# Kernel optimization log

Hardware: AMD Instinct MI355X
Metric: run time of the kernel (lower is better)

Reference implementation:

```python
import jax, jax.numpy as jnp
import numpy as np

N_NODES = 50000
N_EDGES = 800000
N_GRAPHS = 64
FEAT = 128
HID = 256
ACT = 32


def setup_inputs() -> dict:
    key = jax.random.key(0)
    ks = jax.random.split(key, 16)
    x = jax.random.normal(ks[0], (N_NODES, FEAT), dtype=jnp.float32)
    edge_index = jax.random.randint(ks[1], (2, N_EDGES), 0, N_NODES, dtype=jnp.int32)
    # sorted graph assignment covering all graphs (avoids empty segments in mean pool)
    batch = (jnp.arange(N_NODES, dtype=jnp.int32) * N_GRAPHS) // N_NODES
    action = jax.random.normal(ks[2], (N_GRAPHS, ACT), dtype=jnp.float32)

    def lin(k, fan_in, fan_out):
        s = 1.0 / np.sqrt(fan_in)
        kw, kb = jax.random.split(k)
        W = jax.random.uniform(kw, (fan_in, fan_out), jnp.float32, -s, s)
        b = jax.random.uniform(kb, (fan_out,), jnp.float32, -s, s)
        return W, b

    q1_W1, q1_b1 = lin(ks[3], FEAT, HID)
    q1_W2, q1_b2 = lin(ks[4], HID, HID)
    q1_fcW, q1_fcb = lin(ks[5], HID + ACT, 1)
    q2_W1, q2_b1 = lin(ks[6], FEAT, HID)
    q2_W2, q2_b2 = lin(ks[7], HID, HID)
    q2_fcW, q2_fcb = lin(ks[8], HID + ACT, 1)
    return dict(x=x, edge_index=edge_index, batch=batch, action=action,
                q1_W1=q1_W1, q1_b1=q1_b1, q1_W2=q1_W2, q1_b2=q1_b2,
                q1_fcW=q1_fcW, q1_fcb=q1_fcb,
                q2_W1=q2_W1, q2_b1=q2_b1, q2_W2=q2_W2, q2_b2=q2_b2,
                q2_fcW=q2_fcW, q2_fcb=q2_fcb)


def _gcn_conv(x, W, b, src, dst, norm, n_nodes):
    # GCNConv: h = D^-1/2 (A+I) D^-1/2 (x W) + b
    h = x @ W                                    # [N, out]
    msg = h[src] * norm[:, None]                 # [E+N, out] gather
    out = jax.ops.segment_sum(msg, dst, num_segments=n_nodes)  # scatter-add
    return out + b


def _critic_head(x, src, dst, norm, batch, action, W1, b1, W2, b2, fcW, fcb, counts):
    n = x.shape[0]
    h = jax.nn.relu(_gcn_conv(x, W1, b1, src, dst, norm, n))
    h = jax.nn.relu(_gcn_conv(h, W2, b2, src, dst, norm, n))
    pooled = jax.ops.segment_sum(h, batch, num_segments=N_GRAPHS) / counts[:, None]
    q_in = jnp.concatenate([pooled, action], axis=-1)
    return q_in @ fcW + fcb


def reference(x, edge_index, batch, action,
              q1_W1, q1_b1, q1_W2, q1_b2, q1_fcW, q1_fcb,
              q2_W1, q2_b1, q2_W2, q2_b2, q2_fcW, q2_fcb):
    n = x.shape[0]
    # add self-loops (PyG GCNConv default)
    loops = jnp.arange(n, dtype=edge_index.dtype)
    src = jnp.concatenate([edge_index[0], loops])
    dst = jnp.concatenate([edge_index[1], loops])
    deg = jax.ops.segment_sum(jnp.ones_like(dst, x.dtype), dst, num_segments=n)
    dis = jnp.where(deg > 0, jax.lax.rsqrt(deg), 0.0)
    norm = dis[src] * dis[dst]                   # symmetric normalization per edge
    counts = jax.ops.segment_sum(jnp.ones_like(batch, x.dtype), batch,
                                 num_segments=N_GRAPHS)
    q1 = _critic_head(x, src, dst, norm, batch, action,
                      q1_W1, q1_b1, q1_W2, q1_b2, q1_fcW, q1_fcb, counts)
    q2 = _critic_head(x, src, dst, norm, batch, action,
                      q2_W1, q2_b1, q2_W2, q2_b2, q2_fcW, q2_fcb, counts)
    return (q1, q2)
```

## Files before the change

### kernel.cpp

```cpp
#include <hip/hip_runtime.h>
#include <hip/hip_bf16.h>

#define FEAT 128
#define HID  256
#define ACTD 32

typedef __attribute__((ext_vector_type(8))) short bf16x8;
typedef __attribute__((ext_vector_type(4))) float f32x4;
typedef __attribute__((ext_vector_type(2))) float f32x2;

__device__ __forceinline__ ushort f2b(float f) {
    __hip_bfloat16 h = __float2bfloat16(f);
    return *(ushort*)&h;
}
__device__ __forceinline__ uint pack2(float lo, float hi) {
    return (uint)f2b(lo) | ((uint)f2b(hi) << 16);
}
__device__ __forceinline__ f32x2 upk_lo(uint u) { return __builtin_amdgcn_cvt_pk_f32_fp8(u, false); }
__device__ __forceinline__ f32x2 upk_hi(uint u) { return __builtin_amdgcn_cvt_pk_f32_fp8(u, true); }

__device__ __forceinline__ void add8(float* acc, uint2 g) {
    f32x2 l0 = upk_lo(g.x), h0 = upk_hi(g.x);
    f32x2 l1 = upk_lo(g.y), h1 = upk_hi(g.y);
    acc[0] += l0[0]; acc[1] += l0[1]; acc[2] += h0[0]; acc[3] += h0[1];
    acc[4] += l1[0]; acc[5] += l1[1]; acc[6] += h1[0]; acc[7] += h1[1];
}


__global__ void hist_bounds(const int* __restrict__ dst, int* __restrict__ cnt, int E,
                            const int* __restrict__ batch, int* __restrict__ sg,
                            int* __restrict__ eg, int n) {
    int i = blockIdx.x * blockDim.x + threadIdx.x;
    if (i < E) atomicAdd(&cnt[dst[i]], 1);
    if (i < n) {
        int b = batch[i];
        if (i == 0 || batch[i - 1] != b) sg[b] = i;
        if (i == n - 1 || batch[i + 1] != b) eg[b] = i + 1;
    }
}

__global__ __launch_bounds__(256) void scan_one(const int* __restrict__ cnt,
        int* __restrict__ row_ptr, int* __restrict__ row_end,
        int* __restrict__ fill_pos, float* __restrict__ dis,
        int* __restrict__ ticket, int n) {
    __shared__ int s[256];
    __shared__ int base_sh;
    int t = threadIdx.x;
    int i = blockIdx.x * 256 + t;
    int c = (i < n) ? cnt[i] : 0;
    s[t] = c;
    __syncthreads();
    for (int off = 1; off < 256; off <<= 1) {
        int u = (t >= off) ? s[t - off] : 0;
        __syncthreads();
        s[t] += u;
        __syncthreads();
    }
    if (t == 255) base_sh = atomicAdd(ticket, s[255]);
    __syncthreads();
    if (i < n) {
        int ex = base_sh + s[t] - c;
        row_ptr[i] = ex;
        row_end[i] = ex + c;
        fill_pos[i] = ex;
        dis[i] = rsqrtf((float)c + 1.0f);
    }
}

__global__ void fill_prep(const int* __restrict__ src, const int* __restrict__ dst,
                          int* __restrict__ fill_pos, int* __restrict__ col_idx, int E,
                          const float* __restrict__ x, const float* __restrict__ dis,
                          uchar* __restrict__ xs,
                          const float* __restrict__ W1a, const float* __restrict__ W1b,
                          const float* __restrict__ W2a, const float* __restrict__ W2b,
                          ushort* __restrict__ WT1, uchar* __restrict__ WT2f, int n) {
    int i = blockIdx.x * blockDim.x + threadIdx.x;
    if (i < E) {
        int d = dst[i];
        int pos = atomicAdd(&fill_pos[d], 1);
        col_idx[pos] = src[i];
        return;
    }
    i -= E;
    const int nscale = n * (FEAT / 4);
    if (i < nscale) {
        int v = i >> 5;
        float dv = dis[v] * 8.f;
        float4 f = ((const float4*)x)[i];
        uint p = __builtin_amdgcn_cvt_pk_fp8_f32(f.x * dv, f.y * dv, 0, false);
        p = __builtin_amdgcn_cvt_pk_fp8_f32(f.z * dv, f.w * dv, p, true);
        ((uint*)xs)[i] = p;
        return;
    }
    i -= nscale;
    if (i < 2 * FEAT * HID) {
        int head = i >> 15;
        int rem = i & 32767;
        int k = rem >> 8, nn = rem & 255;
        const float* W = head ? W1b : W1a;
        WT1[(size_t)(head * 256 + nn) * FEAT + k] = f2b(W[rem]);
    } else {
        int j = i - 2 * FEAT * HID;
        if (j >= 2 * HID * HID) return;
        int head = j >> 16;
        int rem = j & 65535;
        int k = rem >> 8, nn = rem & 255;
        const float* W = head ? W2b : W2a;
        float v = W[rem] * 8.f;
        uint q = __builtin_amdgcn_cvt_pk_fp8_f32(v, v, 0, false);
        WT2f[(size_t)head * 65536 + nn * 256 + k] = (uchar)(q & 0xff);
    }
}


__global__ __launch_bounds__(256) void agg128(
        const uchar* __restrict__ xs, const float* __restrict__ dis,
        const int* __restrict__ row_ptr, const int* __restrict__ row_end,
        const int* __restrict__ col_idx,
        ushort* __restrict__ z, int n) {
    const int wave = threadIdx.x >> 6, lane = threadIdx.x & 63;
    const int v = blockIdx.x * 4 + wave;
    if (v >= n) return;
    const ushort* X = (const ushort*)xs;
    f32x2 p = upk_lo((uint)X[(size_t)v * 64 + lane]);
    float a0 = p[0], a1 = p[1];
    const int e0 = row_ptr[v], e1 = row_end[v];
    int e = e0;
    for (; e + 8 <= e1; e += 8) {
        uint m[8];
#pragma unroll
        for (int j = 0; j < 8; ++j) m[j] = X[(size_t)col_idx[e + j] * 64 + lane];
#pragma unroll
        for (int j = 0; j < 8; ++j) {
            f32x2 q = upk_lo(m[j]);
            a0 += q[0]; a1 += q[1];
        }
    }
    for (; e < e1; ++e) {
        f32x2 m = upk_lo((uint)X[(size_t)col_idx[e] * 64 + lane]);
        a0 += m[0]; a1 += m[1];
    }
    float sc = dis[v] * 0.125f;
    ((uint*)z)[(size_t)v * 64 + lane] = pack2(a0 * sc, a1 * sc);
}


__global__ __launch_bounds__(256) void agg512(
        const uchar* __restrict__ h1, const float* __restrict__ dis,
        const int* __restrict__ row_ptr, const int* __restrict__ row_end,
        const int* __restrict__ col_idx,
        uchar* __restrict__ z2f, int n) {
    const int wave = threadIdx.x >> 6, lane = threadIdx.x & 63;
    const int v = blockIdx.x * 4 + wave;
    if (v >= n) return;
    const uint2* H = (const uint2*)h1;
    float acc[8];
    {
        uint2 g = H[(size_t)v * 64 + lane];
        f32x2 l0 = upk_lo(g.x), h0 = upk_hi(g.x);
        f32x2 l1 = upk_lo(g.y), h1v = upk_hi(g.y);
        acc[0] = l0[0]; acc[1] = l0[1]; acc[2] = h0[0]; acc[3] = h0[1];
        acc[4] = l1[0]; acc[5] = l1[1]; acc[6] = h1v[0]; acc[7] = h1v[1];
    }
    const int e0 = row_ptr[v], e1 = row_end[v];
    int e = e0;
    for (; e + 8 <= e1; e += 8) {
        uint2 m[8];
#pragma unroll
        for (int j = 0; j < 8; ++j) m[j] = H[(size_t)col_idx[e + j] * 64 + lane];
#pragma unroll
        for (int j = 0; j < 8; ++j) add8(acc, m[j]);
    }
    for (; e < e1; ++e) add8(acc, H[(size_t)col_idx[e] * 64 + lane]);
    float sc = dis[v] * 0.25f;
    uint lo = __builtin_amdgcn_cvt_pk_fp8_f32(acc[0] * sc, acc[1] * sc, 0, false);
    lo = __builtin_amdgcn_cvt_pk_fp8_f32(acc[2] * sc, acc[3] * sc, lo, true);
    uint hi = __builtin_amdgcn_cvt_pk_fp8_f32(acc[4] * sc, acc[5] * sc, 0, false);
    hi = __builtin_amdgcn_cvt_pk_fp8_f32(acc[6] * sc, acc[7] * sc, hi, true);
    uint2 o = {lo, hi};
    ((uint2*)z2f)[(size_t)v * 64 + lane] = o;
}


__global__ __launch_bounds__(512) void gemm1_mfma(
        const ushort* __restrict__ z,
        const ushort* __restrict__ WT1,
        const float* __restrict__ b1a, const float* __restrict__ b1b,
        const float* __restrict__ dis,
        uchar* __restrict__ out, int M) {
    constexpr int K = FEAT;
    __shared__ char Bs[256 * 256];
    const int tid = threadIdx.x;
    const int bm = blockIdx.x * 128;
    const int head = blockIdx.y;
    const ushort* WT = WT1 + (size_t)head * 256 * K;
    const float* bias = head ? b1b : b1a;

    for (int idx = tid; idx < 256 * 16; idx += 512) {
        int nr = idx >> 4, seg = idx & 15;
        int4 val = *(const int4*)(WT + (size_t)nr * K + seg * 8);
        int byte = (nr * 256 + seg * 16) ^ ((nr & 7) << 4);
        *(int4*)(Bs + byte) = val;
    }
    __syncthreads();

    const int warp = tid >> 6, lane = tid & 63;
    const int wr = warp >> 1, wc = warp & 1;
    const int kgrp = lane >> 4;
    const int r0 = wr * 32 + (lane & 15);
    const int c0 = wc * 128 + (lane & 15);

    f32x4 acc[2][8] = {};
    const bf16x8 zv = {};
    for (int ks = 0; ks < 4; ++ks) {
        bf16x8 a[2], b[8];
#pragma unroll
        for (int m = 0; m < 2; ++m) {
            int grow = bm + r0 + m * 16;
            a[m] = (grow < M)
                 ? *(const bf16x8*)(z + (size_t)grow * K + ks * 32 + kgrp * 8)
                 : zv;
        }
#pragma unroll
        for (int nf = 0; nf < 8; ++nf) {
            int nr = c0 + nf * 16;
            int byte = (nr * 256 + ks * 64 + kgrp * 16) ^ ((nr & 7) << 4);
            b[nf] = *(const bf16x8*)(Bs + byte);
        }
#pragma unroll
        for (int nf = 0; nf < 8; ++nf)
#pragma unroll
            for (int m = 0; m < 2; ++m)
                acc[m][nf] = __builtin_amdgcn_mfma_f32_16x16x32_bf16(b[nf], a[m], acc[m][nf], 0, 0, 0);
    }

    const int ml = lane & 15;
    const int ngrp = (lane >> 4) * 4;
#pragma unroll
    for (int m = 0; m < 2; ++m) {
        int grow = bm + wr * 32 + m * 16 + ml;
        if (grow >= M) continue;
        float d = dis[grow] * 16.f;
#pragma unroll
        for (int nf = 0; nf < 8; ++nf) {
            int n0 = wc * 128 + nf * 16 + ngrp;
            float4 bv = *(const float4*)(bias + n0);
            f32x4 ac = acc[m][nf];
            float v0 = fmaxf(ac[0] + bv.x, 0.f) * d;
            float v1 = fmaxf(ac[1] + bv.y, 0.f) * d;
            float v2 = fmaxf(ac[2] + bv.z, 0.f) * d;
            float v3 = fmaxf(ac[3] + bv.w, 0.f) * d;
            uint q = __builtin_amdgcn_cvt_pk_fp8_f32(v0, v1, 0, false);
            q = __builtin_amdgcn_cvt_pk_fp8_f32(v2, v3, q, true);
            *(uint*)(out + (size_t)grow * 512 + head * 256 + n0) = q;
        }
    }
}


__global__ __launch_bounds__(512) void gemm2_pool(
        const uchar* __restrict__ z2f,
        const uchar* __restrict__ WT2f,
        const float* __restrict__ b2a, const float* __restrict__ b2b,
        const int* __restrict__ batch,
        float* __restrict__ pooled, int M) {
    constexpr int K = HID;
    __shared__ char Bs[256 * 256];
    __shared__ int rows_g[128];
    const int tid = threadIdx.x;
    const int bm = blockIdx.x * 128;
    const int head = blockIdx.y;
    const uchar* WT = WT2f + (size_t)head * 65536;
    const float* bias = head ? b2b : b2a;

    for (int idx = tid; idx < 256 * 32; idx += 512) {
        int nr = idx >> 5, seg = idx & 31;
        uint2 val = *(const uint2*)(WT + (size_t)nr * 256 + seg * 8);
        int byte = (nr * 256 + seg * 8) ^ ((nr & 7) << 3);
        *(uint2*)(Bs + byte) = val;
    }
    if (tid < 128) rows_g[tid] = batch[min(bm + tid, M - 1)];
    __syncthreads();

    const int warp = tid >> 6, lane = tid & 63;
    const int wr = warp >> 1, wc = warp & 1;
    const int kgrp = lane >> 4;
    const int r0 = wr * 32 + (lane & 15);
    const int c0 = wc * 128 + (lane & 15);
    const uchar* Abase = z2f + (size_t)head * 256;

    f32x4 acc[2][8] = {};
    for (int ks = 0; ks < 8; ++ks) {
        long a[2], b[8];
#pragma unroll
        for (int m = 0; m < 2; ++m) {
            int grow = bm + r0 + m * 16;
            a[m] = (grow < M)
                 ? *(const long*)(Abase + (size_t)grow * 512 + ks * 32 + kgrp * 8)
                 : 0L;
        }
#pragma unroll
        for (int nf = 0; nf < 8; ++nf) {
            int nr = c0 + nf * 16;
            int byte = (nr * 256 + ks * 32 + kgrp * 8) ^ ((nr & 7) << 3);
            b[nf] = *(const long*)(Bs + byte);
        }
#pragma unroll
        for (int nf = 0; nf < 8; ++nf)
#pragma unroll
            for (int m = 0; m < 2; ++m)
                acc[m][nf] = __builtin_amdgcn_mfma_f32_16x16x32_fp8_fp8(a[m], b[nf], acc[m][nf], 0, 0, 0);
    }

    const int rbw = wr * 32;
    const int g0 = rows_g[rbw];
    const int glast = rows_g[min(127, rbw + 31)];
    float s0[8] = {}, s1[8] = {};
#pragma unroll
    for (int m = 0; m < 2; ++m) {
#pragma unroll
        for (int r = 0; r < 4; ++r) {
            int lrow = rbw + m * 16 + (lane >> 4) * 4 + r;
            int grow = bm + lrow;
            if (grow < M) {
                bool in0 = (rows_g[lrow] == g0);
#pragma unroll
                for (int nf = 0; nf < 8; ++nf) {
                    float val = fmaxf(acc[m][nf][r] * 0.03125f + bias[c0 + nf * 16], 0.f);
                    if (in0) s0[nf] += val; else s1[nf] += val;
                }
            }
        }
    }
#pragma unroll
    for (int nf = 0; nf < 8; ++nf) {
        s0[nf] += __shfl_xor(s0[nf], 16, 64);
        s0[nf] += __shfl_xor(s0[nf], 32, 64);
        s1[nf] += __shfl_xor(s1[nf], 16, 64);
        s1[nf] += __shfl_xor(s1[nf], 32, 64);
    }
    if (kgrp == 0) {
#pragma unroll
        for (int nf = 0; nf < 8; ++nf) {
            int n = head * 256 + c0 + nf * 16;
            atomicAdd(&pooled[(size_t)g0 * 512 + n], s0[nf]);
            if (glast != g0) atomicAdd(&pooled[(size_t)glast * 512 + n], s1[nf]);
        }
    }
}

__global__ __launch_bounds__(512) void final_dot(
        const float* __restrict__ pooled, const int* __restrict__ sg,
        const int* __restrict__ eg, const float* __restrict__ action,
        const float* __restrict__ fcW1, const float* __restrict__ fcb1,
        const float* __restrict__ fcW2, const float* __restrict__ fcb2,
        float* __restrict__ out, int G) {
    int g = blockIdx.x, t = threadIdx.x;
    int head = t >> 8, f = t & 255;
    const float* fcW = head ? fcW2 : fcW1;
    float inv = 1.f / (float)(eg[g] - sg[g]);
    float p = pooled[g * 512 + t] * inv * fcW[f];
    if (f < ACTD) p += action[g * ACTD + f] * fcW[HID + f];
    for (int off = 32; off; off >>= 1) p += __shfl_down(p, off, 64);
    __shared__ float red[8];
    if ((t & 63) == 0) red[t >> 6] = p;
    __syncthreads();
    if (t == 0)   out[g]     = red[0] + red[1] + red[2] + red[3] + fcb1[0];
    if (t == 256) out[G + g] = red[4] + red[5] + red[6] + red[7] + fcb2[0];
}


extern "C" void kernel_launch(void* const* d_in, const int* in_sizes, int n_in,
                              void* d_out, int out_size, void* d_ws, size_t ws_size,
                              hipStream_t stream) {
    const float* x      = (const float*)d_in[0];
    const int*   ei     = (const int*)d_in[1];
    const int*   batch  = (const int*)d_in[2];
    const float* action = (const float*)d_in[3];
    const float* q1_W1  = (const float*)d_in[4];
    const float* q1_b1  = (const float*)d_in[5];
    const float* q1_W2  = (const float*)d_in[6];
    const float* q1_b2  = (const float*)d_in[7];
    const float* q1_fcW = (const float*)d_in[8];
    const float* q1_fcb = (const float*)d_in[9];
    const float* q2_W1  = (const float*)d_in[10];
    const float* q2_b1  = (const float*)d_in[11];
    const float* q2_W2  = (const float*)d_in[12];
    const float* q2_b2  = (const float*)d_in[13];
    const float* q2_fcW = (const float*)d_in[14];
    const float* q2_fcb = (const float*)d_in[15];

    const int N = in_sizes[2];
    const int E = in_sizes[1] / 2;
    const int G = in_sizes[3] / ACTD;
    const int* src = ei;
    const int* dst = ei + E;

    char* w = (char*)d_ws;
    size_t off = 0;
    auto take = [&](size_t bytes) -> void* {
        void* p = w + off;
        off = (off + bytes + 255) & ~(size_t)255;
        return p;
    };
    int*    cnt      = (int*)take((size_t)(N + 1) * 4);
    int*    row_ptr  = (int*)take((size_t)N * 4);
    int*    row_end  = (int*)take((size_t)N * 4);
    int*    fill_pos = (int*)take((size_t)N * 4);
    float*  dis      = (float*)take((size_t)N * 4);
    int*    col_idx  = (int*)take((size_t)E * 4);
    int*    sg       = (int*)take((size_t)G * 4);
    int*    eg       = (int*)take((size_t)G * 4);
    ushort* WT1      = (ushort*)take((size_t)512 * FEAT * 2);
    uchar*  WT2f     = (uchar*)take((size_t)2 * HID * HID);
    float*  pooled   = (float*)take((size_t)G * 512 * 4);
    uchar*  xs       = (uchar*)take((size_t)N * FEAT);
    ushort* z        = (ushort*)take((size_t)N * FEAT * 2);
    uchar*  h1       = (uchar*)take((size_t)N * 512);
    uchar*  z2f      = (uchar*)take((size_t)N * 512);
    (void)ws_size;

    const int TB = 256;
    const int nb = (N + 255) / 256;
    hipMemsetAsync(cnt, 0, (size_t)(N + 1) * 4, stream);
    hipMemsetAsync(pooled, 0, (size_t)G * 512 * 4, stream);

    int hb_grid = (max(E, N) + TB - 1) / TB;
    hist_bounds<<<hb_grid, TB, 0, stream>>>(dst, cnt, E, batch, sg, eg, N);
    scan_one<<<nb, TB, 0, stream>>>(cnt, row_ptr, row_end, fill_pos, dis, cnt + N, N);

    int fptotal = E + N * (FEAT / 4) + 2 * FEAT * HID + 2 * HID * HID;
    fill_prep<<<(fptotal + TB - 1) / TB, TB, 0, stream>>>(
        src, dst, fill_pos, col_idx, E,
        x, dis, xs, q1_W1, q2_W1, q1_W2, q2_W2, WT1, WT2f, N);

    int agg_grid = (N + 3) / 4;
    int gx128 = (N + 127) / 128;

    agg128<<<agg_grid, TB, 0, stream>>>(xs, dis, row_ptr, row_end, col_idx, z, N);
    gemm1_mfma<<<dim3(gx128, 2), 512, 0, stream>>>(z, WT1, q1_b1, q2_b1, dis, h1, N);
    agg512<<<agg_grid, TB, 0, stream>>>(h1, dis, row_ptr, row_end, col_idx, z2f, N);
    gemm2_pool<<<dim3(gx128, 2), 512, 0, stream>>>(z2f, WT2f, q1_b2, q2_b2, batch,
                                                   pooled, N);
    final_dot<<<G, 512, 0, stream>>>(pooled, sg, eg, action,
                                     q1_fcW, q1_fcb, q2_fcW, q2_fcb,
                                     (float*)d_out, G);
}
```

Before: 269.1 us.

## Fuse preprocessing kernels into one persistent kernel with grid barriers

Merges the histogram, scan and CSR-fill/quantize kernels into a single persistent kernel of 784 blocks that uses atomic-counter grid barriers between phases. It also places cnt and pooled next to each other so one memset clears both plus the barrier counters. The aim is to remove two kernel launches and one memset. The cost is spin-wait barriers, which depend on all 784 blocks being resident at once, and grid-stride loops that may lower per-phase parallelism.

Measured after the change: 516.1 us. 91.8% more time.

```diff
diff --git a/kernel.cpp b/kernel.cpp
--- a/kernel.cpp
+++ b/kernel.cpp
@@ -4,6 +4,7 @@
 #define FEAT 128
 #define HID  256
 #define ACTD 32
+#define NBP  784
 
 typedef __attribute__((ext_vector_type(8))) short bf16x8;
 typedef __attribute__((ext_vector_type(4))) float f32x4;
@@ -26,89 +27,103 @@
     acc[4] += l1[0]; acc[5] += l1[1]; acc[6] += h1[0]; acc[7] += h1[1];
 }
 
-
-__global__ void hist_bounds(const int* __restrict__ dst, int* __restrict__ cnt, int E,
-                            const int* __restrict__ batch, int* __restrict__ sg,
-                            int* __restrict__ eg, int n) {
-    int i = blockIdx.x * blockDim.x + threadIdx.x;
-    if (i < E) atomicAdd(&cnt[dst[i]], 1);
-    if (i < n) {
+__device__ __forceinline__ void gbar(int* ctr, int target) {
+    __syncthreads();
+    if (threadIdx.x == 0) {
+        __threadfence();
+        atomicAdd(ctr, 1);
+        while (atomicAdd(ctr, 0) < target) __builtin_amdgcn_s_sleep(2);
+    }
+    __syncthreads();
+    __threadfence();
+}
+
+
+__global__ __launch_bounds__(256) void preproc(
+        const int* __restrict__ src, const int* __restrict__ dst,
+        const int* __restrict__ batch,
+        int* __restrict__ cnt, int* __restrict__ sg, int* __restrict__ eg,
+        int* __restrict__ row_ptr, int* __restrict__ row_end,
+        int* __restrict__ fill_pos, float* __restrict__ dis,
+        int* __restrict__ col_idx,
+        const float* __restrict__ x, uchar* __restrict__ xs,
+        const float* __restrict__ W1a, const float* __restrict__ W1b,
+        const float* __restrict__ W2a, const float* __restrict__ W2b,
+        ushort* __restrict__ WT1, uchar* __restrict__ WT2f,
+        int E, int n) {
+    const int tid = threadIdx.x, bid = blockIdx.x;
+    const int gsz = NBP * 256;
+    const int gi = bid * 256 + tid;
+    int* ticket = cnt + n;
+    int* bar0 = cnt + n + 1;
+    int* bar1 = cnt + n + 2;
+
+    for (int i = gi; i < E; i += gsz) atomicAdd(&cnt[dst[i]], 1);
+    for (int i = gi; i < n; i += gsz) {
         int b = batch[i];
         if (i == 0 || batch[i - 1] != b) sg[b] = i;
         if (i == n - 1 || batch[i + 1] != b) eg[b] = i + 1;
     }
-}
-
-__global__ __launch_bounds__(256) void scan_one(const int* __restrict__ cnt,
-        int* __restrict__ row_ptr, int* __restrict__ row_end,
-        int* __restrict__ fill_pos, float* __restrict__ dis,
-        int* __restrict__ ticket, int n) {
-    __shared__ int s[256];
-    __shared__ int base_sh;
-    int t = threadIdx.x;
-    int i = blockIdx.x * 256 + t;
-    int c = (i < n) ? cnt[i] : 0;
-    s[t] = c;
-    __syncthreads();
-    for (int off = 1; off < 256; off <<= 1) {
-        int u = (t >= off) ? s[t - off] : 0;
+    const int wtot = 2 * FEAT * HID + 2 * HID * HID;
+    for (int i = gi; i < wtot; i += gsz) {
+        if (i < 2 * FEAT * HID) {
+            int head = i >> 15;
+            int rem = i & 32767;
+            int k = rem >> 8, nn = rem & 255;
+            const float* W = head ? W1b : W1a;
+            WT1[(size_t)(head * 256 + nn) * FEAT + k] = f2b(W[rem]);
+        } else {
+            int j = i - 2 * FEAT * HID;
+            int head = j >> 16;
+            int rem = j & 65535;
+            int k = rem >> 8, nn = rem & 255;
+            const float* W = head ? W2b : W2a;
+            float v = W[rem] * 8.f;
+            uint q = __builtin_amdgcn_cvt_pk_fp8_f32(v, v, 0, false);
+            WT2f[(size_t)head * 65536 + nn * 256 + k] = (uchar)(q & 0xff);
+        }
+    }
+    gbar(bar0, NBP);
+
+    const int nbs = (n + 255) >> 8;
+    if (bid < nbs) {
+        __shared__ int s[256];
+        __shared__ int base_sh;
+        int i = bid * 256 + tid;
+        int c = (i < n) ? cnt[i] : 0;
+        s[tid] = c;
         __syncthreads();
-        s[t] += u;
+        for (int off = 1; off < 256; off <<= 1) {
+            int u = (tid >= off) ? s[tid - off] : 0;
+            __syncthreads();
+            s[tid] += u;
+            __syncthreads();
+        }
+        if (tid == 255) base_sh = atomicAdd(ticket, s[255]);
         __syncthreads();
-    }
-    if (t == 255) base_sh = atomicAdd(ticket, s[255]);
-    __syncthreads();
-    if (i < n) {
-        int ex = base_sh + s[t] - c;
-        row_ptr[i] = ex;
-        row_end[i] = ex + c;
-        fill_pos[i] = ex;
-        dis[i] = rsqrtf((float)c + 1.0f);
-    }
-}
-
-__global__ void fill_prep(const int* __restrict__ src, const int* __restrict__ dst,
-                          int* __restrict__ fill_pos, int* __restrict__ col_idx, int E,
-                          const float* __restrict__ x, const float* __restrict__ dis,
-                          uchar* __restrict__ xs,
-                          const float* __restrict__ W1a, const float* __restrict__ W1b,
-                          const float* __restrict__ W2a, const float* __restrict__ W2b,
-                          ushort* __restrict__ WT1, uchar* __restrict__ WT2f, int n) {
-    int i = blockIdx.x * blockDim.x + threadIdx.x;
-    if (i < E) {
+        if (i < n) {
+            int ex = base_sh + s[tid] - c;
+            row_ptr[i] = ex;
+            row_end[i] = ex + c;
+            fill_pos[i] = ex;
+            dis[i] = rsqrtf((float)c + 1.0f);
+        }
+    }
+    gbar(bar1, NBP);
+
+    for (int i = gi; i < E; i += gsz) {
         int d = dst[i];
         int pos = atomicAdd(&fill_pos[d], 1);
         col_idx[pos] = src[i];
-        return;
-    }
-    i -= E;
+    }
     const int nscale = n * (FEAT / 4);
-    if (i < nscale) {
+    for (int i = gi; i < nscale; i += gsz) {
         int v = i >> 5;
         float dv = dis[v] * 8.f;
         float4 f = ((const float4*)x)[i];
         uint p = __builtin_amdgcn_cvt_pk_fp8_f32(f.x * dv, f.y * dv, 0, false);
         p = __builtin_amdgcn_cvt_pk_fp8_f32(f.z * dv, f.w * dv, p, true);
         ((uint*)xs)[i] = p;
-        return;
-    }
-    i -= nscale;
-    if (i < 2 * FEAT * HID) {
-        int head = i >> 15;
-        int rem = i & 32767;
-        int k = rem >> 8, nn = rem & 255;
-        const float* W = head ? W1b : W1a;
-        WT1[(size_t)(head * 256 + nn) * FEAT + k] = f2b(W[rem]);
-    } else {
-        int j = i - 2 * FEAT * HID;
-        if (j >= 2 * HID * HID) return;
-        int head = j >> 16;
-        int rem = j & 65535;
-        int k = rem >> 8, nn = rem & 255;
-        const float* W = head ? W2b : W2a;
-        float v = W[rem] * 8.f;
-        uint q = __builtin_amdgcn_cvt_pk_fp8_f32(v, v, 0, false);
-        WT2f[(size_t)head * 65536 + nn * 256 + k] = (uchar)(q & 0xff);
     }
 }
 
@@ -403,7 +418,8 @@
         off = (off + bytes + 255) & ~(size_t)255;
         return p;
     };
-    int*    cnt      = (int*)take((size_t)(N + 1) * 4);
+    int*    cnt      = (int*)take((size_t)(N + 3) * 4);
+    float*  pooled   = (float*)take((size_t)G * 512 * 4);
     int*    row_ptr  = (int*)take((size_t)N * 4);
     int*    row_end  = (int*)take((size_t)N * 4);
     int*    fill_pos = (int*)take((size_t)N * 4);
@@ -413,7 +429,6 @@
     int*    eg       = (int*)take((size_t)G * 4);
     ushort* WT1      = (ushort*)take((size_t)512 * FEAT * 2);
     uchar*  WT2f     = (uchar*)take((size_t)2 * HID * HID);
-    float*  pooled   = (float*)take((size_t)G * 512 * 4);
     uchar*  xs       = (uchar*)take((size_t)N * FEAT);
     ushort* z        = (ushort*)take((size_t)N * FEAT * 2);
     uchar*  h1       = (uchar*)take((size_t)N * 512);
@@ -421,18 +436,14 @@
     (void)ws_size;
 
     const int TB = 256;
-    const int nb = (N + 255) / 256;
-    hipMemsetAsync(cnt, 0, (size_t)(N + 1) * 4, stream);
-    hipMemsetAsync(pooled, 0, (size_t)G * 512 * 4, stream);
-
-    int hb_grid = (max(E, N) + TB - 1) / TB;
-    hist_bounds<<<hb_grid, TB, 0, stream>>>(dst, cnt, E, batch, sg, eg, N);
-    scan_one<<<nb, TB, 0, stream>>>(cnt, row_ptr, row_end, fill_pos, dis, cnt + N, N);
-
-    int fptotal = E + N * (FEAT / 4) + 2 * FEAT * HID + 2 * HID * HID;
-    fill_prep<<<(fptotal + TB - 1) / TB, TB, 0, stream>>>(
-        src, dst, fill_pos, col_idx, E,
-        x, dis, xs, q1_W1, q2_W1, q1_W2, q2_W2, WT1, WT2f, N);
+    size_t zlen = (size_t)((char*)pooled - (char*)cnt) + (size_t)G * 512 * 4;
+    hipMemsetAsync(cnt, 0, zlen, stream);
+
+    preproc<<<NBP, TB, 0, stream>>>(src, dst, batch,
+                                    cnt, sg, eg, row_ptr, row_end, fill_pos, dis,
+                                    col_idx, x, xs,
+                                    q1_W1, q2_W1, q1_W2, q2_W2, WT1, WT2f,
+                                    E, N);
 
     int agg_grid = (N + 3) / 4;
     int gx128 = (N + 127) / 128;
```
